# Optimization experiments

Measured on AMD Instinct MI355X. Metric: run time of the kernel, lower is better.

Reference implementation:

```python
import jax, jax.numpy as jnp
import numpy as np

N_NODES = 8192
N_EDGES = 524288
N_PAIRS = 262144
N_TYPES = 86


def _gcn_conv(x, W, b, src, dst, n):
    # PyG GCNConv: transform, add self-loops, symmetric degree normalization,
    # scatter-add aggregation at destination nodes.
    xw = x @ W  # [N, F_out]
    loop = jnp.arange(n, dtype=src.dtype)
    s = jnp.concatenate([src, loop])
    d = jnp.concatenate([dst, loop])
    deg = jax.ops.segment_sum(jnp.ones(d.shape, xw.dtype), d, num_segments=n)
    dinv = jnp.where(deg > 0, jax.lax.rsqrt(deg), 0.0)  # deg^{-1/2}, 0 for isolated
    coef = dinv[s] * dinv[d]  # [E+N]
    out = jax.ops.segment_sum(xw[s] * coef[:, None], d, num_segments=n)
    return out + b


def setup_inputs() -> dict:
    key = jax.random.key(0)
    ks = jax.random.split(key, 10)
    x = jax.random.normal(ks[0], (N_NODES, N_NODES), dtype=jnp.float32)
    edge_index = jax.random.randint(ks[1], (2, N_EDGES), 0, N_NODES, dtype=jnp.int32)
    drug1_idx = jax.random.randint(ks[2], (N_PAIRS,), 0, N_NODES, dtype=jnp.int32)
    drug2_idx = jax.random.randint(ks[3], (N_PAIRS,), 0, N_NODES, dtype=jnp.int32)
    W1 = jax.random.normal(ks[4], (N_NODES, 128), dtype=jnp.float32) / np.sqrt(N_NODES)
    b1 = jnp.zeros((128,), jnp.float32)
    W2 = jax.random.normal(ks[5], (128, 64), dtype=jnp.float32) / np.sqrt(128.0)
    b2 = jnp.zeros((64,), jnp.float32)
    Wfc = jax.random.normal(ks[6], (128, N_TYPES), dtype=jnp.float32) / np.sqrt(128.0)
    bfc = jnp.zeros((N_TYPES,), jnp.float32)
    return {"x": x, "edge_index": edge_index, "drug1_idx": drug1_idx,
            "drug2_idx": drug2_idx, "W1": W1, "b1": b1, "W2": W2, "b2": b2,
            "Wfc": Wfc, "bfc": bfc}


def reference(x, edge_index, drug1_idx, drug2_idx, W1, b1, W2, b2, Wfc, bfc):
    n = x.shape[0]
    src, dst = edge_index[0], edge_index[1]
    h = jax.nn.relu(_gcn_conv(x, W1, b1, src, dst, n))
    # dropout p=0.3 is identity at inference (training=False)
    h = jax.nn.relu(_gcn_conv(h, W2, b2, src, dst, n))
    combined = jnp.concatenate([h[drug1_idx], h[drug2_idx]], axis=1)  # [P, 128]
    return jax.nn.sigmoid(combined @ Wfc + bfc)
```

## Files before the change

### kernel.cpp

```cpp
#include <hip/hip_runtime.h>
#include <math.h>
#include <stdint.h>
#include <stddef.h>

#define N_NODES 8192
#define N_EDGES 524288
#define N_PAIRS 262144
#define N_TYPES 86
#define F1 128
#define F2 64

typedef unsigned short ushort_t;
typedef unsigned int uint_t;
typedef __attribute__((ext_vector_type(8))) short bfrag;
typedef __attribute__((ext_vector_type(4))) float ffrag;

typedef __attribute__((address_space(3))) char lds_char;
typedef __attribute__((address_space(1))) const char g_char;

__device__ __forceinline__ void gload16(const void* g, void* l) {
  __builtin_amdgcn_global_load_lds((const g_char*)g, (lds_char*)l, 16, 0, 0);
}

__device__ inline ushort_t f2bf(float f) {
  uint_t u = __float_as_uint(f);
  uint_t r = u + 0x7fffu + ((u >> 16) & 1u);
  return (ushort_t)(r >> 16);
}
__device__ inline float bf2f(ushort_t h) {
  return __uint_as_float(((uint_t)h) << 16);
}


__global__ void zero_k(int* __restrict__ p) {
  p[blockIdx.x * 256 + threadIdx.x] = 0;
}

__global__ void count_deg_k(const int* __restrict__ dst, int* __restrict__ cnt) {
  int e = blockIdx.x * blockDim.x + threadIdx.x;
  if (e < N_EDGES) atomicAdd(&cnt[dst[e]], 1);
}

__global__ void scan_k(const int* __restrict__ cnt, int* __restrict__ rp,
                       int* __restrict__ fill, float* __restrict__ dinv) {
  __shared__ int s[1024];
  int t = threadIdx.x;
  int v[8];
  int sum = 0;
#pragma unroll
  for (int i = 0; i < 8; i++) {
    v[i] = cnt[t * 8 + i];
    dinv[t * 8 + i] = 1.0f / sqrtf((float)(v[i] + 1));
    sum += v[i];
  }
  s[t] = sum;
  __syncthreads();
  for (int off = 1; off < 1024; off <<= 1) {
    int add = (t >= off) ? s[t - off] : 0;
    __syncthreads();
    s[t] += add;
    __syncthreads();
  }
  int excl = s[t] - sum;
#pragma unroll
  for (int i = 0; i < 8; i++) {
    rp[t * 8 + i] = excl;
    fill[t * 8 + i] = excl;
    excl += v[i];
  }
  if (t == 1023) rp[N_NODES] = excl;
}

__global__ void scatter_k(const int* __restrict__ src, const int* __restrict__ dst,
                          int* fill, int* __restrict__ csr) {
  int e = blockIdx.x * blockDim.x + threadIdx.x;
  if (e < N_EDGES) {
    int d = dst[e];
    int pos = atomicAdd(&fill[d], 1);
    csr[pos] = src[e];
  }
}


__global__ __launch_bounds__(256) void w1split_k(const float* __restrict__ W1,
                                                 ushort_t* __restrict__ W1th,
                                                 ushort_t* __restrict__ W1tl) {
  __shared__ ushort_t lh[32 * 65];
  __shared__ ushort_t ll[32 * 65];
  int tid = threadIdx.x;
  int k0 = blockIdx.x * 64;
  int n0 = blockIdx.y * 32;
#pragma unroll
  for (int i = 0; i < 8; i++) {
    int c = tid + 256 * i;
    int kr = c >> 5, nc = c & 31;
    float v = W1[(size_t)(k0 + kr) * F1 + n0 + nc];
    ushort_t h = f2bf(v);
    ushort_t l = f2bf(v - bf2f(h));
    lh[nc * 65 + kr] = h;
    ll[nc * 65 + kr] = l;
  }
  __syncthreads();
#pragma unroll
  for (int i = 0; i < 2; i++) {
    int c = tid + 256 * i;
    int buf = c >> 8;
    int cc = c & 255;
    int nr = cc >> 3, kc = cc & 7;
    const ushort_t* l = buf ? ll : lh;
    uint4 u;
    u.x = (uint_t)l[nr * 65 + kc * 8 + 0] | ((uint_t)l[nr * 65 + kc * 8 + 1] << 16);
    u.y = (uint_t)l[nr * 65 + kc * 8 + 2] | ((uint_t)l[nr * 65 + kc * 8 + 3] << 16);
    u.z = (uint_t)l[nr * 65 + kc * 8 + 4] | ((uint_t)l[nr * 65 + kc * 8 + 5] << 16);
    u.w = (uint_t)l[nr * 65 + kc * 8 + 6] | ((uint_t)l[nr * 65 + kc * 8 + 7] << 16);
    ushort_t* dst = (buf ? W1tl : W1th) + (size_t)(n0 + nr) * N_NODES + k0 + kc * 8;
    *(uint4*)dst = u;
  }
}


#define AWB(b) ((b) * 65536)
#define BBB(b) (131072 + (b) * 16384)

#define SCHED0 __builtin_amdgcn_sched_barrier(0)
#define WAITVM(N)  do { asm volatile("s_waitcnt vmcnt(" #N ")" ::: "memory"); SCHED0; } while (0)
#define WAITVML(N) do { asm volatile("s_waitcnt vmcnt(" #N ") lgkmcnt(0)" ::: "memory"); SCHED0; } while (0)

__global__ __launch_bounds__(512) void gemm1_mfma_k(const float* __restrict__ x,
                                                    const ushort_t* __restrict__ W1th,
                                                    const ushort_t* __restrict__ W1tl,
                                                    float* __restrict__ part) {
  __shared__ __align__(16) char lds[163840];
  int tid = threadIdx.x;
  int wave = tid >> 6, lane = tid & 63;
  int wr = wave >> 2, wc = wave & 3;
  int lrow = lane & 15, kgrp = lane >> 4;
  int m_blk = blockIdx.y * 64;
  int kbase = blockIdx.x * 4096;

  const ushort_t* bsrc = (wave < 4) ? W1th : W1tl;
  int b_half = (wave < 4) ? 0 : 8192;
  int bq = wave & 3;
  int b_row = bq * 32 + (lane >> 2);
  int b_kel = ((lane & 3) ^ ((lane >> 2) & 3)) << 3;

  ffrag acc[2][2];
#pragma unroll
  for (int mi = 0; mi < 2; mi++)
#pragma unroll
    for (int ni = 0; ni < 2; ni++) acc[mi][ni] = (ffrag)(0.0f);

  float4 ch[3];

#define ISSUE_B(K0, BSEL)                                                            \
  {                                                                                  \
    _Pragma("unroll") for (int i = 0; i < 2; i++) {                                  \
      const ushort_t* gp = bsrc + (size_t)(b_row + i * 16) * N_NODES + (K0) + b_kel; \
      gload16(gp, lds + BBB(BSEL) + b_half + bq * 2048 + i * 1024);                  \
    }                                                                                \
  }

#define ISSUE_A(J, KW)                                                               \
  ch[(J) % 3] = *(const float4*)&x[(size_t)(m_blk + wave * 8 + (J)) * N_NODES + (KW) + lane * 4];

#define CONV_A(J, BSEL)                                                              \
  {                                                                                  \
    float4 v = ch[(J) % 3];                                                          \
    int r = wave * 8 + (J);                                                          \
    ushort_t h0 = f2bf(v.x), h1 = f2bf(v.y), h2 = f2bf(v.z), h3 = f2bf(v.w);         \
    ushort_t l0 = f2bf(v.x - bf2f(h0)), l1 = f2bf(v.y - bf2f(h1));                   \
    ushort_t l2 = f2bf(v.z - bf2f(h2)), l3 = f2bf(v.w - bf2f(h3));                   \
    uint2 hp, lp;                                                                    \
    hp.x = (uint_t)h0 | ((uint_t)h1 << 16); hp.y = (uint_t)h2 | ((uint_t)h3 << 16);  \
    lp.x = (uint_t)l0 | ((uint_t)l1 << 16); lp.y = (uint_t)l2 | ((uint_t)l3 << 16);  \
    uint_t off = r * 512 + ((((lane >> 1) ^ (r & 15))) << 4) + ((lane & 1) << 3);    \
    *(uint2*)(lds + AWB(BSEL) + off) = hp;                                           \
    *(uint2*)(lds + AWB(BSEL) + 32768 + off) = lp;                                   \
  }

#define COMPUTE(S, ASEL)                                                             \
  {                                                                                  \
    bfrag bh[2], bl[2];                                                              \
    _Pragma("unroll") for (int ni = 0; ni < 2; ni++) {                               \
      int brow = wc * 32 + ni * 16 + lrow;                                           \
      uint_t boff = brow * 64 + ((kgrp * 16) ^ ((brow & 3) << 4));                   \
      bh[ni] = *(const bfrag*)(lds + BBB((S) & 1) + boff);                           \
      bl[ni] = *(const bfrag*)(lds + BBB((S) & 1) + 8192 + boff);                    \
    }                                                                                \
    _Pragma("unroll") for (int mi = 0; mi < 2; mi++) {                               \
      int arow = wr * 32 + mi * 16 + lrow;                                           \
      uint_t aoff = arow * 512 + ((((S) * 4 + kgrp) ^ (arow & 15)) << 4);            \
      bfrag ah = *(const bfrag*)(lds + AWB(ASEL) + aoff);                            \
      bfrag al = *(const bfrag*)(lds + AWB(ASEL) + 32768 + aoff);                    \
      _Pragma("unroll") for (int ni = 0; ni < 2; ni++) {                             \
        acc[mi][ni] = __builtin_amdgcn_mfma_f32_16x16x32_bf16(ah, bh[ni], acc[mi][ni], 0, 0, 0); \
        acc[mi][ni] = __builtin_amdgcn_mfma_f32_16x16x32_bf16(ah, bl[ni], acc[mi][ni], 0, 0, 0); \
        acc[mi][ni] = __builtin_amdgcn_mfma_f32_16x16x32_bf16(al, bh[ni], acc[mi][ni], 0, 0, 0); \
      }                                                                              \
    }                                                                                \
  }

  ISSUE_B(kbase, 0);
  SCHED0;
  {
    float4 ch8[8];
#pragma unroll
    for (int j = 0; j < 8; j++)
      ch8[j] = *(const float4*)&x[(size_t)(m_blk + wave * 8 + j) * N_NODES + kbase + lane * 4];
    WAITVML(0);
#pragma unroll
    for (int j = 0; j < 8; j++) {
      float4 v = ch8[j];
      int r = wave * 8 + j;
      ushort_t h0 = f2bf(v.x), h1 = f2bf(v.y), h2 = f2bf(v.z), h3 = f2bf(v.w);
      ushort_t l0 = f2bf(v.x - bf2f(h0)), l1 = f2bf(v.y - bf2f(h1));
      ushort_t l2 = f2bf(v.z - bf2f(h2)), l3 = f2bf(v.w - bf2f(h3));
      uint2 hp, lp;
      hp.x = (uint_t)h0 | ((uint_t)h1 << 16); hp.y = (uint_t)h2 | ((uint_t)h3 << 16);
      lp.x = (uint_t)l0 | ((uint_t)l1 << 16); lp.y = (uint_t)l2 | ((uint_t)l3 << 16);
      uint_t off = r * 512 + ((((lane >> 1) ^ (r & 15))) << 4) + ((lane & 1) << 3);
      *(uint2*)(lds + AWB(0) + off) = hp;
      *(uint2*)(lds + AWB(0) + 32768 + off) = lp;
    }
  }
  asm volatile("s_waitcnt lgkmcnt(0)" ::: "memory");
  SCHED0;
  __builtin_amdgcn_s_barrier();
  SCHED0;

  for (int w = 0; w < 16; ++w) {
    const int awc = w & 1, awn = (w + 1) & 1;
    const int wns = (w < 15) ? (w + 1) : 15;
    const int kw = kbase + w * 256;
    const int kwn = kbase + wns * 256;
#pragma unroll
    for (int s = 0; s < 8; ++s) {
      int kbn = (s < 7) ? (kw + (s + 1) * 32) : kwn;
      ISSUE_B(kbn, (s + 1) & 1);
      SCHED0;
      if (s == 0) { ISSUE_A(0, kwn); ISSUE_A(1, kwn); }
      else if (s < 7) { ISSUE_A(s + 1, kwn); }
      SCHED0;
      __builtin_amdgcn_s_setprio(1);
      COMPUTE(s, awc);
      __builtin_amdgcn_s_setprio(0);
      if (s >= 1 && s <= 6) {
        WAITVM(3);
        CONV_A(s - 1, awn);
      } else if (s == 7) {
        WAITVM(2);
        CONV_A(6, awn);
        CONV_A(7, awn);
      }
      if (s == 0) { WAITVML(2); }
      else if (s < 7) { WAITVML(1); }
      else { WAITVML(0); }
      __builtin_amdgcn_s_barrier();
      SCHED0;
    }
  }

  float* outp = part + (size_t)blockIdx.x * (N_NODES * F1);
#pragma unroll
  for (int mi = 0; mi < 2; mi++) {
#pragma unroll
    for (int ni = 0; ni < 2; ni++) {
      int col = wc * 32 + ni * 16 + lrow;
#pragma unroll
      for (int r = 0; r < 4; r++) {
        int row = m_blk + wr * 32 + mi * 16 + kgrp * 4 + r;
        outp[(size_t)row * F1 + col] = acc[mi][ni][r];
      }
    }
  }
#undef ISSUE_B
#undef ISSUE_A
#undef CONV_A
#undef COMPUTE
}

__global__ void reduceS_k(const float* __restrict__ part, float* __restrict__ xw1, int S) {
  int i = blockIdx.x * blockDim.x + threadIdx.x;
  float4 a = ((const float4*)part)[i];
  for (int s = 1; s < S; s++) {
    float4 b = ((const float4*)(part + (size_t)s * N_NODES * F1))[i];
    a.x += b.x; a.y += b.y; a.z += b.z; a.w += b.w;
  }
  ((float4*)xw1)[i] = a;
}


template <int F>
__global__ void agg_k(const float* __restrict__ xw, const int* __restrict__ csr,
                      const int* __restrict__ rp, const float* __restrict__ dinv,
                      const float* __restrict__ bias, float* __restrict__ hout) {
  int node = blockIdx.x;
  int f = threadIdx.x;
  __shared__ int sidx[F];
  __shared__ float sdv[F];
  int beg = rp[node], end = rp[node + 1];
  float acc = 0.f;
  for (int base = beg; base < end; base += F) {
    int n = end - base;
    if (n > F) n = F;
    __syncthreads();
    if (f < n) {
      int s = csr[base + f];
      sidx[f] = s;
      sdv[f] = dinv[s];
    }
    __syncthreads();
    for (int i = 0; i < n; i++) acc += xw[(size_t)sidx[i] * F + f] * sdv[i];
  }
  float dv = dinv[node];
  float v = (acc + xw[(size_t)node * F + f] * dv) * dv + bias[f];
  hout[(size_t)node * F + f] = v > 0.f ? v : 0.f;
}


__global__ __launch_bounds__(256) void gemm2_k(const float* __restrict__ h1,
                                               const float* __restrict__ W2,
                                               float* __restrict__ xw2) {
  __shared__ float W2s[F1 * F2];
  __shared__ float As[16 * F1];
  int tid = threadIdx.x;
  int r0 = blockIdx.x * 16;
#pragma unroll
  for (int j = 0; j < 8; j++)
    ((float4*)W2s)[tid + 256 * j] = ((const float4*)W2)[tid + 256 * j];
#pragma unroll
  for (int j = 0; j < 2; j++)
    ((float4*)As)[tid + 256 * j] = ((const float4*)(h1 + (size_t)r0 * F1))[tid + 256 * j];
  __syncthreads();
  int r = tid >> 4, c4 = tid & 15;
  float4 acc = make_float4(0.f, 0.f, 0.f, 0.f);
#pragma unroll 8
  for (int k = 0; k < F1; k++) {
    float a = As[r * F1 + k];
    float4 bv = *(float4*)&W2s[k * F2 + 4 * c4];
    acc.x += a * bv.x; acc.y += a * bv.y; acc.z += a * bv.z; acc.w += a * bv.w;
  }
  *(float4*)&xw2[(size_t)(r0 + r) * F2 + 4 * c4] = acc;
}


__global__ void pboth_k(const float* __restrict__ h2, const float* __restrict__ Wfc,
                        float* __restrict__ P) {
  __shared__ float hs[64 * 16];
  int tid = threadIdx.x;
  int r0 = blockIdx.x * 16;
  for (int idx = tid; idx < 256; idx += 192) {
    int row = idx >> 4, k4 = idx & 15;
    float4 h = *(const float4*)&h2[(size_t)(r0 + row) * F2 + 4 * k4];
    hs[(4 * k4 + 0) * 16 + row] = h.x;
    hs[(4 * k4 + 1) * 16 + row] = h.y;
    hs[(4 * k4 + 2) * 16 + row] = h.z;
    hs[(4 * k4 + 3) * 16 + row] = h.w;
  }
  __syncthreads();
  if (tid < 172) {
    int half = tid < 86 ? 0 : 1;
    int j = tid - 86 * half;
    const float* wp = Wfc + (size_t)(64 * half) * N_TYPES + j;
    float acc[16];
#pragma unroll
    for (int r = 0; r < 16; r++) acc[r] = 0.f;
    for (int k = 0; k < 64; k++) {
      float w = wp[(size_t)k * N_TYPES];
      const float* hk = &hs[k * 16];
#pragma unroll
      for (int r = 0; r < 16; r++) acc[r] += hk[r] * w;
    }
#pragma unroll
    for (int r = 0; r < 16; r++) P[(size_t)(r0 + r) * 172 + tid] = acc[r];
  }
}


__global__ void final_k(const float* __restrict__ P, const int* __restrict__ d1,
                        const int* __restrict__ d2, const float* __restrict__ bfc,
                        float* __restrict__ out) {
  int gid = blockIdx.x * blockDim.x + threadIdx.x;
  if (gid >= N_PAIRS * 43) return;
  int p = gid / 43;
  int j = gid - p * 43;
  int a = d1[p], b = d2[p];
  float2 v1 = *(const float2*)&P[(size_t)a * 172 + 2 * j];
  float2 v2 = *(const float2*)&P[(size_t)b * 172 + 86 + 2 * j];
  float2 bb = *(const float2*)&bfc[2 * j];
  float z0 = v1.x + v2.x + bb.x;
  float z1 = v1.y + v2.y + bb.y;
  float2 o;
  o.x = 1.0f / (1.0f + expf(-z0));
  o.y = 1.0f / (1.0f + expf(-z1));
  *(float2*)&out[(size_t)p * 86 + 2 * j] = o;
}


extern "C" void kernel_launch(void* const* d_in, const int* in_sizes, int n_in,
                              void* d_out, int out_size, void* d_ws, size_t ws_size,
                              hipStream_t stream) {
  const float* x   = (const float*)d_in[0];
  const int*   ei  = (const int*)d_in[1];
  const int*   d1  = (const int*)d_in[2];
  const int*   d2  = (const int*)d_in[3];
  const float* W1  = (const float*)d_in[4];
  const float* b1  = (const float*)d_in[5];
  const float* W2  = (const float*)d_in[6];
  const float* b2  = (const float*)d_in[7];
  const float* Wfc = (const float*)d_in[8];
  const float* bfc = (const float*)d_in[9];
  float* out = (float*)d_out;

  const int* esrc = ei;
  const int* edst = ei + N_EDGES;

  char* w = (char*)d_ws;
  size_t off = 0;
  auto alloc = [&](size_t bytes) -> char* {
    char* p = w + off;
    off += (bytes + 255) & ~(size_t)255;
    return p;
  };
  int*      cnt  = (int*)alloc((size_t)N_NODES * 4);
  float*    dinv = (float*)alloc((size_t)N_NODES * 4);
  int*      rp   = (int*)alloc((size_t)(N_NODES + 1) * 4);
  int*      fill = (int*)alloc((size_t)N_NODES * 4);
  int*      csr  = (int*)alloc((size_t)N_EDGES * 4);
  ushort_t* W1th = (ushort_t*)alloc((size_t)N_NODES * F1 * 2);
  ushort_t* W1tl = (ushort_t*)alloc((size_t)N_NODES * F1 * 2);
  float*    h1   = (float*)alloc((size_t)N_NODES * F1 * 4);
  float*    xw2  = (float*)alloc((size_t)N_NODES * F2 * 4);
  float*    h2   = (float*)alloc((size_t)N_NODES * F2 * 4);
  float*    P    = (float*)alloc((size_t)N_NODES * 172 * 4);

  const int S = 2;
  size_t partBytes = (size_t)N_NODES * F1 * 4;
  float* part = (float*)alloc((size_t)S * partBytes);
  float* xw1 = part;
  if (off > ws_size) return;

  zero_k<<<N_NODES / 256, 256, 0, stream>>>(cnt);
  count_deg_k<<<N_EDGES / 256, 256, 0, stream>>>(edst, cnt);
  scan_k<<<1, 1024, 0, stream>>>(cnt, rp, fill, dinv);
  scatter_k<<<N_EDGES / 256, 256, 0, stream>>>(esrc, edst, fill, csr);

  w1split_k<<<dim3(N_NODES / 64, F1 / 32), 256, 0, stream>>>(W1, W1th, W1tl);
  gemm1_mfma_k<<<dim3(S, N_NODES / 64), 512, 0, stream>>>(x, W1th, W1tl, part);
  reduceS_k<<<(N_NODES * F1 / 4) / 256, 256, 0, stream>>>(part, xw1, S);
  agg_k<F1><<<N_NODES, F1, 0, stream>>>(xw1, csr, rp, dinv, b1, h1);

  gemm2_k<<<N_NODES / 16, 256, 0, stream>>>(h1, W2, xw2);
  agg_k<F2><<<N_NODES, F2, 0, stream>>>(xw2, csr, rp, dinv, b2, h2);

  pboth_k<<<N_NODES / 16, 192, 0, stream>>>(h2, Wfc, P);
  final_k<<<(N_PAIRS * 43 + 255) / 256, 256, 0, stream>>>(P, d1, d2, bfc, out);
}
```

Baseline: 293.7 us.

## Shrink gemm1 block to 256 threads with small LDS and raise split-K

Rewrites the split-bf16 MFMA GEMM for x@W1 to use 4 waves per block with a 40KB LDS footprint, in place of 8 waves and 160KB. Each wave now computes 32x64 of the output, and the block double-buffers only B while staging one 32-wide A tile per step. The split-K factor rises from 2 to up to 8 depending on workspace size, so the kernel runs more blocks at higher occupancy. The cost is more partial-sum traffic in the reduction, an extra barrier per k-step, and loss of the deep A prefetch pipeline.

Result: faster. 286.0 us (-2.6%).

```diff
diff --git a/kernel.cpp b/kernel.cpp
--- a/kernel.cpp
+++ b/kernel.cpp
@@ -119,80 +119,91 @@
 }
 
 
-#define AWB(b) ((b) * 65536)
-#define BBB(b) (131072 + (b) * 16384)
+#define OAH 0
+#define OAL 4096
+#define OBB(b) (8192 + (b) * 16384)
 
 #define SCHED0 __builtin_amdgcn_sched_barrier(0)
 #define WAITVM(N)  do { asm volatile("s_waitcnt vmcnt(" #N ")" ::: "memory"); SCHED0; } while (0)
 #define WAITVML(N) do { asm volatile("s_waitcnt vmcnt(" #N ") lgkmcnt(0)" ::: "memory"); SCHED0; } while (0)
 
-__global__ __launch_bounds__(512) void gemm1_mfma_k(const float* __restrict__ x,
-                                                    const ushort_t* __restrict__ W1th,
-                                                    const ushort_t* __restrict__ W1tl,
-                                                    float* __restrict__ part) {
-  __shared__ __align__(16) char lds[163840];
+__global__ __launch_bounds__(256, 4) void gemm1_mfma_k(const float* __restrict__ x,
+                                                       const ushort_t* __restrict__ W1th,
+                                                       const ushort_t* __restrict__ W1tl,
+                                                       float* __restrict__ part, int kspan) {
+  __shared__ __align__(16) char lds[40960];
   int tid = threadIdx.x;
   int wave = tid >> 6, lane = tid & 63;
-  int wr = wave >> 2, wc = wave & 3;
+  int wr = wave >> 1, wc = wave & 1;
   int lrow = lane & 15, kgrp = lane >> 4;
   int m_blk = blockIdx.y * 64;
-  int kbase = blockIdx.x * 4096;
-
-  const ushort_t* bsrc = (wave < 4) ? W1th : W1tl;
-  int b_half = (wave < 4) ? 0 : 8192;
-  int bq = wave & 3;
+  int kbase = blockIdx.x * kspan;
+  int ktiles = kspan >> 5;
+
+  int bq = wave;
   int b_row = bq * 32 + (lane >> 2);
   int b_kel = ((lane & 3) ^ ((lane >> 2) & 3)) << 3;
 
-  ffrag acc[2][2];
+  ffrag acc[2][4];
 #pragma unroll
   for (int mi = 0; mi < 2; mi++)
 #pragma unroll
-    for (int ni = 0; ni < 2; ni++) acc[mi][ni] = (ffrag)(0.0f);
-
-  float4 ch[3];
+    for (int ni = 0; ni < 4; ni++) acc[mi][ni] = (ffrag)(0.0f);
+
+  float4 av[2];
+
+#define LOADA(K0)                                                                    \
+  {                                                                                  \
+    _Pragma("unroll") for (int i = 0; i < 2; i++) {                                  \
+      int c = tid + 256 * i;                                                         \
+      int row = c >> 3, c4 = c & 7;                                                  \
+      av[i] = *(const float4*)&x[(size_t)(m_blk + row) * N_NODES + (K0) + 4 * c4];   \
+    }                                                                                \
+  }
 
 #define ISSUE_B(K0, BSEL)                                                            \
   {                                                                                  \
     _Pragma("unroll") for (int i = 0; i < 2; i++) {                                  \
-      const ushort_t* gp = bsrc + (size_t)(b_row + i * 16) * N_NODES + (K0) + b_kel; \
-      gload16(gp, lds + BBB(BSEL) + b_half + bq * 2048 + i * 1024);                  \
+      const ushort_t* gh = W1th + (size_t)(b_row + i * 16) * N_NODES + (K0) + b_kel; \
+      gload16(gh, lds + OBB(BSEL) + bq * 2048 + i * 1024);                           \
+      const ushort_t* gl = W1tl + (size_t)(b_row + i * 16) * N_NODES + (K0) + b_kel; \
+      gload16(gl, lds + OBB(BSEL) + 8192 + bq * 2048 + i * 1024);                    \
     }                                                                                \
   }
 
-#define ISSUE_A(J, KW)                                                               \
-  ch[(J) % 3] = *(const float4*)&x[(size_t)(m_blk + wave * 8 + (J)) * N_NODES + (KW) + lane * 4];
-
-#define CONV_A(J, BSEL)                                                              \
+#define STOREA()                                                                     \
   {                                                                                  \
-    float4 v = ch[(J) % 3];                                                          \
-    int r = wave * 8 + (J);                                                          \
-    ushort_t h0 = f2bf(v.x), h1 = f2bf(v.y), h2 = f2bf(v.z), h3 = f2bf(v.w);         \
-    ushort_t l0 = f2bf(v.x - bf2f(h0)), l1 = f2bf(v.y - bf2f(h1));                   \
-    ushort_t l2 = f2bf(v.z - bf2f(h2)), l3 = f2bf(v.w - bf2f(h3));                   \
-    uint2 hp, lp;                                                                    \
-    hp.x = (uint_t)h0 | ((uint_t)h1 << 16); hp.y = (uint_t)h2 | ((uint_t)h3 << 16);  \
-    lp.x = (uint_t)l0 | ((uint_t)l1 << 16); lp.y = (uint_t)l2 | ((uint_t)l3 << 16);  \
-    uint_t off = r * 512 + ((((lane >> 1) ^ (r & 15))) << 4) + ((lane & 1) << 3);    \
-    *(uint2*)(lds + AWB(BSEL) + off) = hp;                                           \
-    *(uint2*)(lds + AWB(BSEL) + 32768 + off) = lp;                                   \
-  }
-
-#define COMPUTE(S, ASEL)                                                             \
+    _Pragma("unroll") for (int i = 0; i < 2; i++) {                                  \
+      int c = tid + 256 * i;                                                         \
+      int row = c >> 3, c4 = c & 7;                                                  \
+      float f0 = av[i].x, f1 = av[i].y, f2 = av[i].z, f3 = av[i].w;                  \
+      ushort_t h0 = f2bf(f0), h1 = f2bf(f1), h2 = f2bf(f2), h3 = f2bf(f3);           \
+      ushort_t l0 = f2bf(f0 - bf2f(h0)), l1 = f2bf(f1 - bf2f(h1));                   \
+      ushort_t l2 = f2bf(f2 - bf2f(h2)), l3 = f2bf(f3 - bf2f(h3));                   \
+      uint2 hp, lp;                                                                  \
+      hp.x = (uint_t)h0 | ((uint_t)h1 << 16); hp.y = (uint_t)h2 | ((uint_t)h3 << 16);\
+      lp.x = (uint_t)l0 | ((uint_t)l1 << 16); lp.y = (uint_t)l2 | ((uint_t)l3 << 16);\
+      uint_t off = row * 64 + ((c4 * 8) ^ ((row & 3) << 4));                         \
+      *(uint2*)(lds + OAH + off) = hp;                                               \
+      *(uint2*)(lds + OAL + off) = lp;                                               \
+    }                                                                                \
+  }
+
+#define COMPUTE(BSEL)                                                                \
   {                                                                                  \
-    bfrag bh[2], bl[2];                                                              \
-    _Pragma("unroll") for (int ni = 0; ni < 2; ni++) {                               \
-      int brow = wc * 32 + ni * 16 + lrow;                                           \
+    bfrag bh[4], bl[4];                                                              \
+    _Pragma("unroll") for (int ni = 0; ni < 4; ni++) {                               \
+      int brow = wc * 64 + ni * 16 + lrow;                                           \
       uint_t boff = brow * 64 + ((kgrp * 16) ^ ((brow & 3) << 4));                   \
-      bh[ni] = *(const bfrag*)(lds + BBB((S) & 1) + boff);                           \
-      bl[ni] = *(const bfrag*)(lds + BBB((S) & 1) + 8192 + boff);                    \
+      bh[ni] = *(const bfrag*)(lds + OBB(BSEL) + boff);                              \
+      bl[ni] = *(const bfrag*)(lds + OBB(BSEL) + 8192 + boff);                       \
     }                                                                                \
     _Pragma("unroll") for (int mi = 0; mi < 2; mi++) {                               \
       int arow = wr * 32 + mi * 16 + lrow;                                           \
-      uint_t aoff = arow * 512 + ((((S) * 4 + kgrp) ^ (arow & 15)) << 4);            \
-      bfrag ah = *(const bfrag*)(lds + AWB(ASEL) + aoff);                            \
-      bfrag al = *(const bfrag*)(lds + AWB(ASEL) + 32768 + aoff);                    \
-      _Pragma("unroll") for (int ni = 0; ni < 2; ni++) {                             \
+      uint_t aoff = arow * 64 + ((kgrp * 16) ^ ((arow & 3) << 4));                   \
+      bfrag ah = *(const bfrag*)(lds + OAH + aoff);                                  \
+      bfrag al = *(const bfrag*)(lds + OAL + aoff);                                  \
+      _Pragma("unroll") for (int ni = 0; ni < 4; ni++) {                             \
         acc[mi][ni] = __builtin_amdgcn_mfma_f32_16x16x32_bf16(ah, bh[ni], acc[mi][ni], 0, 0, 0); \
         acc[mi][ni] = __builtin_amdgcn_mfma_f32_16x16x32_bf16(ah, bl[ni], acc[mi][ni], 0, 0, 0); \
         acc[mi][ni] = __builtin_amdgcn_mfma_f32_16x16x32_bf16(al, bh[ni], acc[mi][ni], 0, 0, 0); \
@@ -200,61 +211,32 @@
     }                                                                                \
   }
 
+  LOADA(kbase);
   ISSUE_B(kbase, 0);
-  SCHED0;
-  {
-    float4 ch8[8];
-#pragma unroll
-    for (int j = 0; j < 8; j++)
-      ch8[j] = *(const float4*)&x[(size_t)(m_blk + wave * 8 + j) * N_NODES + kbase + lane * 4];
-    WAITVML(0);
-#pragma unroll
-    for (int j = 0; j < 8; j++) {
-      float4 v = ch8[j];
-      int r = wave * 8 + j;
-      ushort_t h0 = f2bf(v.x), h1 = f2bf(v.y), h2 = f2bf(v.z), h3 = f2bf(v.w);
-      ushort_t l0 = f2bf(v.x - bf2f(h0)), l1 = f2bf(v.y - bf2f(h1));
-      ushort_t l2 = f2bf(v.z - bf2f(h2)), l3 = f2bf(v.w - bf2f(h3));
-      uint2 hp, lp;
-      hp.x = (uint_t)h0 | ((uint_t)h1 << 16); hp.y = (uint_t)h2 | ((uint_t)h3 << 16);
-      lp.x = (uint_t)l0 | ((uint_t)l1 << 16); lp.y = (uint_t)l2 | ((uint_t)l3 << 16);
-      uint_t off = r * 512 + ((((lane >> 1) ^ (r & 15))) << 4) + ((lane & 1) << 3);
-      *(uint2*)(lds + AWB(0) + off) = hp;
-      *(uint2*)(lds + AWB(0) + 32768 + off) = lp;
-    }
-  }
-  asm volatile("s_waitcnt lgkmcnt(0)" ::: "memory");
-  SCHED0;
+  WAITVM(4);
+  STOREA();
+  WAITVML(0);
   __builtin_amdgcn_s_barrier();
   SCHED0;
 
-  for (int w = 0; w < 16; ++w) {
-    const int awc = w & 1, awn = (w + 1) & 1;
-    const int wns = (w < 15) ? (w + 1) : 15;
-    const int kw = kbase + w * 256;
-    const int kwn = kbase + wns * 256;
-#pragma unroll
-    for (int s = 0; s < 8; ++s) {
-      int kbn = (s < 7) ? (kw + (s + 1) * 32) : kwn;
-      ISSUE_B(kbn, (s + 1) & 1);
+  for (int s = 0; s < ktiles; ++s) {
+    int more = (s + 1 < ktiles);
+    if (more) {
+      int k0n = kbase + ((s + 1) << 5);
+      LOADA(k0n);
       SCHED0;
-      if (s == 0) { ISSUE_A(0, kwn); ISSUE_A(1, kwn); }
-      else if (s < 7) { ISSUE_A(s + 1, kwn); }
+      ISSUE_B(k0n, (s + 1) & 1);
       SCHED0;
-      __builtin_amdgcn_s_setprio(1);
-      COMPUTE(s, awc);
-      __builtin_amdgcn_s_setprio(0);
-      if (s >= 1 && s <= 6) {
-        WAITVM(3);
-        CONV_A(s - 1, awn);
-      } else if (s == 7) {
-        WAITVM(2);
-        CONV_A(6, awn);
-        CONV_A(7, awn);
-      }
-      if (s == 0) { WAITVML(2); }
-      else if (s < 7) { WAITVML(1); }
-      else { WAITVML(0); }
+    }
+    __builtin_amdgcn_s_setprio(1);
+    COMPUTE(s & 1);
+    __builtin_amdgcn_s_setprio(0);
+    __builtin_amdgcn_s_barrier();
+    SCHED0;
+    if (more) {
+      WAITVM(4);
+      STOREA();
+      WAITVML(0);
       __builtin_amdgcn_s_barrier();
       SCHED0;
     }
@@ -264,8 +246,8 @@
 #pragma unroll
   for (int mi = 0; mi < 2; mi++) {
 #pragma unroll
-    for (int ni = 0; ni < 2; ni++) {
-      int col = wc * 32 + ni * 16 + lrow;
+    for (int ni = 0; ni < 4; ni++) {
+      int col = wc * 64 + ni * 16 + lrow;
 #pragma unroll
       for (int r = 0; r < 4; r++) {
         int row = m_blk + wr * 32 + mi * 16 + kgrp * 4 + r;
@@ -273,9 +255,9 @@
       }
     }
   }
+#undef LOADA
 #undef ISSUE_B
-#undef ISSUE_A
-#undef CONV_A
+#undef STOREA
 #undef COMPUTE
 }
 
@@ -434,8 +416,9 @@
   float*    h2   = (float*)alloc((size_t)N_NODES * F2 * 4);
   float*    P    = (float*)alloc((size_t)N_NODES * 172 * 4);
 
-  const int S = 2;
   size_t partBytes = (size_t)N_NODES * F1 * 4;
+  int S = 8;
+  while (S > 1 && off + (size_t)S * partBytes > ws_size) S >>= 1;
   float* part = (float*)alloc((size_t)S * partBytes);
   float* xw1 = part;
   if (off > ws_size) return;
@@ -446,8 +429,9 @@
   scatter_k<<<N_EDGES / 256, 256, 0, stream>>>(esrc, edst, fill, csr);
 
   w1split_k<<<dim3(N_NODES / 64, F1 / 32), 256, 0, stream>>>(W1, W1th, W1tl);
-  gemm1_mfma_k<<<dim3(S, N_NODES / 64), 512, 0, stream>>>(x, W1th, W1tl, part);
-  reduceS_k<<<(N_NODES * F1 / 4) / 256, 256, 0, stream>>>(part, xw1, S);
+  gemm1_mfma_k<<<dim3(S, N_NODES / 64), 256, 0, stream>>>(x, W1th, W1tl, part, N_NODES / S);
+  if (S > 1)
+    reduceS_k<<<(N_NODES * F1 / 4) / 256, 256, 0, stream>>>(part, xw1, S);
   agg_k<F1><<<N_NODES, F1, 0, stream>>>(xw1, csr, rp, dinv, b1, h1);
 
   gemm2_k<<<N_NODES / 16, 256, 0, stream>>>(h1, W2, xw2);
```
